# Kernel optimization log

Measured on AMD Instinct MI355X. Metric: run time of the kernel, lower is better.

The kernel has to match this reference:

```python
import jax, jax.numpy as jnp
import numpy as np


def setup_inputs() -> dict:
    key = jax.random.key(0)
    ks = jax.random.split(key, 7)
    B, H, W, C, HID = 8, 64, 64, 16, 256
    s = 0.05
    return {
        "x": jax.random.normal(ks[0], (B, H, W, C), jnp.float32),
        "W1": jax.random.normal(ks[1], (C, HID), jnp.float32) * s,
        "b1": jax.random.normal(ks[2], (C, HID), jnp.float32) * s,
        "W2": jax.random.normal(ks[3], (C, HID, HID), jnp.float32) * s,
        "b2": jax.random.normal(ks[4], (C, HID), jnp.float32) * s,
        "W3": jax.random.normal(ks[5], (C, HID, 3), jnp.float32) * s,
        "b3": jax.random.normal(ks[6], (C, 3), jnp.float32) * s,
    }


def reference(x, W1, b1, W2, b2, W3, b3):
    # x: [B,H,W,C] -> per-channel independent 3-layer MLP (1 -> HID -> HID -> 3)
    B, H, W, C = x.shape
    xf = x.reshape(-1, C)                                   # [N, C]
    # fc1: Linear(1, HID) per channel == scalar * weight + bias
    h = jax.nn.relu(xf[:, :, None] * W1[None] + b1[None])   # [N, C, HID]
    # fc2: batched GEMM over channels
    h = jax.nn.relu(jnp.einsum('nch,chk->nck', h, W2) + b2[None])  # [N, C, HID]
    # fc3: HID -> 3 per channel
    out = jnp.einsum('nch,cho->nco', h, W3) + b3[None]      # [N, C, 3]
    # torch.cat(outputs, dim=1) yields [c0_0..c0_2, c1_0..c1_2, ...] == reshape
    return out.reshape(B, H, W, C * 3)
```

## Files before the change

### kernel.cpp

```cpp
#include <hip/hip_runtime.h>
#include <hip/hip_bf16.h>


typedef __bf16 bf16_t;
typedef __attribute__((ext_vector_type(8))) __bf16 bf16x8;
typedef __attribute__((ext_vector_type(4))) __bf16 bf16x4;
typedef __attribute__((ext_vector_type(4))) float floatx4;

#define C_CH  16
#define HID   256
#define TILES 16
#define NSEG  257
#define GPTS  4097
#define XLO   (-6.0f)
#define XSTEP (12.0f / 4096.0f)

__device__ __forceinline__ unsigned mword(int i) {
  return 0x9E3779B1u + (unsigned)i * 0x85EBCA77u;
}

__global__ __launch_bounds__(512, 2) void kan_all(
    const float* __restrict__ x,
    const float* __restrict__ W1, const float* __restrict__ b1,
    const float* __restrict__ W2, const float* __restrict__ b2,
    const float* __restrict__ W3, const float* __restrict__ b3,
    bf16_t* __restrict__ tab, float* __restrict__ ftab,
    unsigned* __restrict__ flags, float* __restrict__ out) {
  __shared__ __align__(16) float tk[256];
  __shared__ float sW1[256], sB1[256];
  __shared__ int prank[2][256];
  __shared__ float caS[256], ccS[256];
  __shared__ float part[8][64][9];
  __shared__ float eA[17], eC[17];
  __shared__ int eH[17];
  __shared__ float tls[256];
  __shared__ short sjs[257];
  const int bid = blockIdx.x;
  const int c = bid & 15;
  const int k = bid >> 4;
  const int j0 = (NSEG * k) >> 4;
  const int j1 = (NSEG * (k + 1)) >> 4;
  const int nev = j1 - 1 - j0;
  const int t = threadIdx.x;

  if (t < 256) {
    float w = W1[c * 256 + t], bv = b1[c * 256 + t];
    sW1[t] = w;
    sB1[t] = bv;
    tk[t] = (w != 0.0f) ? (-bv / w) : 3.0e38f;
  }
  __syncthreads();
  {
    const int e = t & 255;
    const int hf = t >> 8;
    const float ke = tk[e];
    const int u0 = hf << 7;
    int r = 0;
#pragma unroll
    for (int uu = 0; uu < 32; ++uu) {
      const int u = u0 + uu * 4;
      const float4 kv = *(const float4*)&tk[u];
      r += (kv.x < ke || (kv.x == ke && (u + 0) < e)) ? 1 : 0;
      r += (kv.y < ke || (kv.y == ke && (u + 1) < e)) ? 1 : 0;
      r += (kv.z < ke || (kv.z == ke && (u + 2) < e)) ? 1 : 0;
      r += (kv.w < ke || (kv.w == ke && (u + 3) < e)) ? 1 : 0;
    }
    prank[hf][e] = r;
  }
  __syncthreads();
  if (t < 256) {
    const int r = prank[0][t] + prank[1][t];
    const float w = sW1[t], bv = sB1[t];
    tls[r] = tk[t];
    if (r >= j0 && r < j0 + nev) {
      const int e = r - j0;
      eA[e] = fabsf(w);
      eC[e] = (w > 0.f) ? bv : ((w < 0.f) ? -bv : 0.f);
      eH[e] = t;
    }
    bool act = (w > 0.f) ? (j0 > r) : ((w < 0.f) ? (j0 <= r) : (bv > 0.f));
    caS[t] = act ? w : 0.f;
    ccS[t] = act ? bv : 0.f;
  }
  __syncthreads();

  const int rg = t >> 6;
  const int q = t & 63;
  const float* W2c = W2 + ((size_t)c << 16);
  {
    float pa0 = 0.f, pa1 = 0.f, pa2 = 0.f, pa3 = 0.f;
    float pc0 = 0.f, pc1 = 0.f, pc2 = 0.f, pc3 = 0.f;
    for (int h0 = rg * 32; h0 < rg * 32 + 32; h0 += 8) {
      float4 v[8];
#pragma unroll
      for (int u = 0; u < 8; ++u)
        v[u] = *(const float4*)(W2c + (size_t)(h0 + u) * 256 + q * 4);
#pragma unroll
      for (int u = 0; u < 8; ++u) {
        float ca = caS[h0 + u], cc = ccS[h0 + u];
        pa0 = fmaf(ca, v[u].x, pa0); pa1 = fmaf(ca, v[u].y, pa1);
        pa2 = fmaf(ca, v[u].z, pa2); pa3 = fmaf(ca, v[u].w, pa3);
        pc0 = fmaf(cc, v[u].x, pc0); pc1 = fmaf(cc, v[u].y, pc1);
        pc2 = fmaf(cc, v[u].z, pc2); pc3 = fmaf(cc, v[u].w, pc3);
      }
    }
    part[rg][q][0] = pa0; part[rg][q][1] = pa1;
    part[rg][q][2] = pa2; part[rg][q][3] = pa3;
    part[rg][q][4] = pc0; part[rg][q][5] = pc1;
    part[rg][q][6] = pc2; part[rg][q][7] = pc3;
  }
  __syncthreads();

  if (t < 256) {
    float accA = 0.f, accC = b2[c * 256 + t];
    {
      const int qq = t >> 2, ii = t & 3;
#pragma unroll
      for (int rr = 0; rr < 8; ++rr) {
        accA += part[rr][qq][ii];
        accC += part[rr][qq][4 + ii];
      }
    }
    {
      bf16_t* rp = tab + ((size_t)c * NSEG + j0) * 512;
      rp[t] = (bf16_t)accA; rp[256 + t] = (bf16_t)accC;
    }

    float ew[16];
#pragma unroll 16
    for (int e = 0; e < 16; ++e)
      if (e < nev) ew[e] = W2c[eH[e] * 256 + t];
#pragma unroll 16
    for (int e = 0; e < 16; ++e) {
      if (e < nev) {
        accA = fmaf(eA[e], ew[e], accA);
        accC = fmaf(eC[e], ew[e], accC);
        bf16_t* rp = tab + ((size_t)c * NSEG + (j0 + 1 + e)) * 512;
        rp[t] = (bf16_t)accA; rp[256 + t] = (bf16_t)accC;
      }
    }
  }

  __syncthreads();
  if (t == 0) {
    __hip_atomic_store(&flags[c * 16 + k], mword(c * 16 + k),
                       __ATOMIC_RELEASE, __HIP_MEMORY_SCOPE_AGENT);
  }
  if (t < 16) {
    const int idx = c * 16 + t;
    const unsigned want = mword(idx);
    while (__hip_atomic_load(&flags[idx], __ATOMIC_RELAXED,
                             __HIP_MEMORY_SCOPE_AGENT) != want) {
      __builtin_amdgcn_s_sleep(4);
    }
  }
  if (t == 0) {
    (void)__hip_atomic_load(&flags[c * 16], __ATOMIC_ACQUIRE,
                            __HIP_MEMORY_SCOPE_AGENT);
  }
  __syncthreads();

  {
    const int gp0 = k << 8;
    const int l16 = t & 15;
    const int g = t >> 4;
    float w3f0[16], w3f1[16], w3f2[16];
#pragma unroll
    for (int u = 0; u < 16; ++u) {
      const float* wp = W3 + ((size_t)c * 256 + l16 * 16 + u) * 3;
      w3f0[u] = wp[0]; w3f1[u] = wp[1]; w3f2[u] = wp[2];
    }
    const float b3v0 = b3[c * 3 + 0], b3v1 = b3[c * 3 + 1], b3v2 = b3[c * 3 + 2];

    if (t < 257) {
      const int gp = gp0 + t;
      if (gp <= 4096) {
        const float xv = XLO + (float)gp * XSTEP;
        int j = 0;
#pragma unroll
        for (int s = 128; s > 0; s >>= 1)
          if (tls[j + s - 1] <= xv) j += s;
        if (j == 255 && tls[255] <= xv) j = 256;
        else if (j < 255 && tls[j] <= xv) ++j;
        sjs[t] = (short)j;
      } else {
        sjs[t] = 0;
      }
    }
    __syncthreads();

    const bf16_t* tabc = tab + (size_t)c * NSEG * 512;
    float xv = XLO + (float)(gp0 + g) * XSTEP;
    const bf16_t* row = tabc + (size_t)sjs[g] * 512 + l16 * 16;
    bf16x8 a0 = *(const bf16x8*)(row);
    bf16x8 a1 = *(const bf16x8*)(row + 8);
    bf16x8 c0 = *(const bf16x8*)(row + 256);
    bf16x8 c1 = *(const bf16x8*)(row + 264);

    for (int i = 0; i < 8; ++i) {
      bf16x8 na0, na1, nc0, nc1;
      float nxv = 0.f;
      if (i < 7) {
        int npl = (i + 1) * 32 + g;
        nxv = XLO + (float)(gp0 + npl) * XSTEP;
        const bf16_t* nrow = tabc + (size_t)sjs[npl] * 512 + l16 * 16;
        na0 = *(const bf16x8*)(nrow);
        na1 = *(const bf16x8*)(nrow + 8);
        nc0 = *(const bf16x8*)(nrow + 256);
        nc1 = *(const bf16x8*)(nrow + 264);
      }
      float s0 = 0.f, s1 = 0.f, s2 = 0.f;
#pragma unroll
      for (int u = 0; u < 8; ++u) {
        float h2 = fmaxf(fmaf(xv, (float)a0[u], (float)c0[u]), 0.f);
        s0 = fmaf(h2, w3f0[u], s0);
        s1 = fmaf(h2, w3f1[u], s1);
        s2 = fmaf(h2, w3f2[u], s2);
      }
#pragma unroll
      for (int u = 0; u < 8; ++u) {
        float h2 = fmaxf(fmaf(xv, (float)a1[u], (float)c1[u]), 0.f);
        s0 = fmaf(h2, w3f0[8 + u], s0);
        s1 = fmaf(h2, w3f1[8 + u], s1);
        s2 = fmaf(h2, w3f2[8 + u], s2);
      }
#pragma unroll
      for (int m = 1; m < 16; m <<= 1) {
        s0 += __shfl_xor(s0, m, 64);
        s1 += __shfl_xor(s1, m, 64);
        s2 += __shfl_xor(s2, m, 64);
      }
      const int gp = gp0 + i * 32 + g;
      if (l16 < 3) {
        float v = (l16 == 0) ? (s0 + b3v0) : (l16 == 1) ? (s1 + b3v1) : (s2 + b3v2);
        ftab[((size_t)c * GPTS + gp) * 4 + l16] = v;
      }
      a0 = na0; a1 = na1; c0 = nc0; c1 = nc1; xv = nxv;
    }

    if (k == 15 && t < 16) {
      const float xvt = XLO + 4096.0f * XSTEP;
      const bf16_t* rowt = tabc + (size_t)sjs[256] * 512 + t * 16;
      bf16x8 ta0 = *(const bf16x8*)(rowt);
      bf16x8 ta1 = *(const bf16x8*)(rowt + 8);
      bf16x8 tc0 = *(const bf16x8*)(rowt + 256);
      bf16x8 tc1 = *(const bf16x8*)(rowt + 264);
      float s0 = 0.f, s1 = 0.f, s2 = 0.f;
#pragma unroll
      for (int u = 0; u < 8; ++u) {
        float h2 = fmaxf(fmaf(xvt, (float)ta0[u], (float)tc0[u]), 0.f);
        s0 = fmaf(h2, w3f0[u], s0);
        s1 = fmaf(h2, w3f1[u], s1);
        s2 = fmaf(h2, w3f2[u], s2);
      }
#pragma unroll
      for (int u = 0; u < 8; ++u) {
        float h2 = fmaxf(fmaf(xvt, (float)ta1[u], (float)tc1[u]), 0.f);
        s0 = fmaf(h2, w3f0[8 + u], s0);
        s1 = fmaf(h2, w3f1[8 + u], s1);
        s2 = fmaf(h2, w3f2[8 + u], s2);
      }
#pragma unroll
      for (int m = 1; m < 16; m <<= 1) {
        s0 += __shfl_xor(s0, m, 64);
        s1 += __shfl_xor(s1, m, 64);
        s2 += __shfl_xor(s2, m, 64);
      }
      if (t < 3) {
        float v = (t == 0) ? (s0 + b3v0) : (t == 1) ? (s1 + b3v1) : (s2 + b3v2);
        ftab[((size_t)c * GPTS + 4096) * 4 + t] = v;
      }
    }
  }

  __syncthreads();
  if (t == 0) {
    __hip_atomic_store(&flags[256 + bid], mword(256 + bid),
                       __ATOMIC_RELEASE, __HIP_MEMORY_SCOPE_AGENT);
  }
  if (t < 256) {
    const int idx = 256 + t;
    const unsigned want = mword(idx);
    while (__hip_atomic_load(&flags[idx], __ATOMIC_RELAXED,
                             __HIP_MEMORY_SCOPE_AGENT) != want) {
      __builtin_amdgcn_s_sleep(4);
    }
  }
  if (t == 0) {
    (void)__hip_atomic_load(&flags[256], __ATOMIC_ACQUIRE,
                            __HIP_MEMORY_SCOPE_AGENT);
  }
  __syncthreads();

  {
    const int base3 = bid * 512 + t;
    const float inv = 1.0f / XSTEP;
    float xv4[4];
#pragma unroll
    for (int it = 0; it < 4; ++it) xv4[it] = x[it * 131072 + base3];
    float4 fa4[4], fb4[4];
    float f4[4];
#pragma unroll
    for (int it = 0; it < 4; ++it) {
      const int flat = it * 131072 + base3;
      const int cc = flat & 15;
      float u = (xv4[it] - XLO) * inv;
      int i = (int)floorf(u);
      i = i < 0 ? 0 : (i > 4095 ? 4095 : i);
      f4[it] = u - (float)i;
      const float4* fp = (const float4*)ftab + (size_t)cc * GPTS + i;
      fa4[it] = fp[0];
      fb4[it] = fp[1];
    }
#pragma unroll
    for (int it = 0; it < 4; ++it) {
      const int flat = it * 131072 + base3;
      float* op = out + (size_t)flat * 3;
      op[0] = fmaf(fb4[it].x - fa4[it].x, f4[it], fa4[it].x);
      op[1] = fmaf(fb4[it].y - fa4[it].y, f4[it], fa4[it].y);
      op[2] = fmaf(fb4[it].z - fa4[it].z, f4[it], fa4[it].z);
    }
  }
}

__global__ __launch_bounds__(512, 2) void build_tab(
    const float* __restrict__ W1, const float* __restrict__ b1,
    const float* __restrict__ W2, const float* __restrict__ b2,
    bf16_t* __restrict__ tab, float* __restrict__ ts_g) {
  __shared__ __align__(16) float tk[256];
  __shared__ float sW1[256], sB1[256];
  __shared__ int prank[2][256];
  __shared__ float caS[256], ccS[256];
  __shared__ float part[8][64][9];
  __shared__ float eA[17], eC[17];
  __shared__ int eH[17];
  const int c = blockIdx.x & 15;
  const int k = blockIdx.x >> 4;
  const int j0 = (NSEG * k) >> 4;
  const int j1 = (NSEG * (k + 1)) >> 4;
  const int nev = j1 - 1 - j0;
  const int t = threadIdx.x;

  if (t < 256) {
    float w = W1[c * 256 + t], bv = b1[c * 256 + t];
    sW1[t] = w;
    sB1[t] = bv;
    tk[t] = (w != 0.0f) ? (-bv / w) : 3.0e38f;
  }
  __syncthreads();
  {
    const int e = t & 255;
    const int hf = t >> 8;
    const float ke = tk[e];
    const int u0 = hf << 7;
    int r = 0;
#pragma unroll
    for (int uu = 0; uu < 32; ++uu) {
      const int u = u0 + uu * 4;
      const float4 kv = *(const float4*)&tk[u];
      r += (kv.x < ke || (kv.x == ke && (u + 0) < e)) ? 1 : 0;
      r += (kv.y < ke || (kv.y == ke && (u + 1) < e)) ? 1 : 0;
      r += (kv.z < ke || (kv.z == ke && (u + 2) < e)) ? 1 : 0;
      r += (kv.w < ke || (kv.w == ke && (u + 3) < e)) ? 1 : 0;
    }
    prank[hf][e] = r;
  }
  __syncthreads();
  if (t < 256) {
    const int r = prank[0][t] + prank[1][t];
    const float w = sW1[t], bv = sB1[t];
    if (k == 0) ts_g[c * 256 + r] = tk[t];
    if (r >= j0 && r < j0 + nev) {
      const int e = r - j0;
      eA[e] = fabsf(w);
      eC[e] = (w > 0.f) ? bv : ((w < 0.f) ? -bv : 0.f);
      eH[e] = t;
    }
    bool act = (w > 0.f) ? (j0 > r) : ((w < 0.f) ? (j0 <= r) : (bv > 0.f));
    caS[t] = act ? w : 0.f;
    ccS[t] = act ? bv : 0.f;
  }
  __syncthreads();

  const int rg = t >> 6;
  const int q = t & 63;
  const float* W2c = W2 + ((size_t)c << 16);
  float pa0 = 0.f, pa1 = 0.f, pa2 = 0.f, pa3 = 0.f;
  float pc0 = 0.f, pc1 = 0.f, pc2 = 0.f, pc3 = 0.f;
  for (int h0 = rg * 32; h0 < rg * 32 + 32; h0 += 8) {
    float4 v[8];
#pragma unroll
    for (int u = 0; u < 8; ++u)
      v[u] = *(const float4*)(W2c + (size_t)(h0 + u) * 256 + q * 4);
#pragma unroll
    for (int u = 0; u < 8; ++u) {
      float ca = caS[h0 + u], cc = ccS[h0 + u];
      pa0 = fmaf(ca, v[u].x, pa0); pa1 = fmaf(ca, v[u].y, pa1);
      pa2 = fmaf(ca, v[u].z, pa2); pa3 = fmaf(ca, v[u].w, pa3);
      pc0 = fmaf(cc, v[u].x, pc0); pc1 = fmaf(cc, v[u].y, pc1);
      pc2 = fmaf(cc, v[u].z, pc2); pc3 = fmaf(cc, v[u].w, pc3);
    }
  }
  part[rg][q][0] = pa0; part[rg][q][1] = pa1;
  part[rg][q][2] = pa2; part[rg][q][3] = pa3;
  part[rg][q][4] = pc0; part[rg][q][5] = pc1;
  part[rg][q][6] = pc2; part[rg][q][7] = pc3;
  __syncthreads();

  if (t < 256) {
    float accA = 0.f, accC = b2[c * 256 + t];
    {
      const int qq = t >> 2, ii = t & 3;
#pragma unroll
      for (int rr = 0; rr < 8; ++rr) {
        accA += part[rr][qq][ii];
        accC += part[rr][qq][4 + ii];
      }
    }
    {
      bf16_t* rp = tab + ((size_t)c * NSEG + j0) * 512;
      rp[t] = (bf16_t)accA; rp[256 + t] = (bf16_t)accC;
    }
    float ew[16];
#pragma unroll 16
    for (int e = 0; e < 16; ++e)
      if (e < nev) ew[e] = W2c[eH[e] * 256 + t];
#pragma unroll 16
    for (int e = 0; e < 16; ++e) {
      if (e < nev) {
        accA = fmaf(eA[e], ew[e], accA);
        accC = fmaf(eC[e], ew[e], accC);
        bf16_t* rp = tab + ((size_t)c * NSEG + (j0 + 1 + e)) * 512;
        rp[t] = (bf16_t)accA; rp[256 + t] = (bf16_t)accC;
      }
    }
  }
}

__global__ __launch_bounds__(256) void build_ftab(
    const bf16_t* __restrict__ tab, const float* __restrict__ ts_g,
    const float* __restrict__ W3, const float* __restrict__ b3,
    float* __restrict__ ftab) {
  __shared__ float tls[256];
  __shared__ short sj[64];
  const int t = threadIdx.x;
  const int c = blockIdx.x & 15;
  const int q = blockIdx.x >> 4;
  const int gp0 = q * 64;

  tls[t] = ts_g[c * 256 + t];

  const int l16 = t & 15;
  const int g = t >> 4;
  float w3f0[16], w3f1[16], w3f2[16];
#pragma unroll
  for (int u = 0; u < 16; ++u) {
    const float* wp = W3 + ((size_t)c * 256 + l16 * 16 + u) * 3;
    w3f0[u] = wp[0]; w3f1[u] = wp[1]; w3f2[u] = wp[2];
  }
  const float b3v0 = b3[c * 3 + 0], b3v1 = b3[c * 3 + 1], b3v2 = b3[c * 3 + 2];
  __syncthreads();

  if (t < 64) {
    const int gp = gp0 + t;
    if (gp <= 4096) {
      const float xv = XLO + (float)gp * XSTEP;
      int j = 0;
#pragma unroll
      for (int s = 128; s > 0; s >>= 1)
        if (tls[j + s - 1] <= xv) j += s;
      if (j == 255 && tls[255] <= xv) j = 256;
      else if (j < 255 && tls[j] <= xv) ++j;
      sj[t] = (short)j;
    } else {
      sj[t] = 0;
    }
  }
  __syncthreads();

  const bf16_t* tabc = tab + (size_t)c * NSEG * 512;
  float xv = XLO + (float)(gp0 + g) * XSTEP;
  const bf16_t* row = tabc + (size_t)sj[g] * 512 + l16 * 16;
  bf16x8 a0 = *(const bf16x8*)(row);
  bf16x8 a1 = *(const bf16x8*)(row + 8);
  bf16x8 c0 = *(const bf16x8*)(row + 256);
  bf16x8 c1 = *(const bf16x8*)(row + 264);

  for (int i = 0; i < 4; ++i) {
    bf16x8 na0, na1, nc0, nc1;
    float nxv = 0.f;
    if (i < 3) {
      int npl = (i + 1) * 16 + g;
      nxv = XLO + (float)(gp0 + npl) * XSTEP;
      const bf16_t* nrow = tabc + (size_t)sj[npl] * 512 + l16 * 16;
      na0 = *(const bf16x8*)(nrow);
      na1 = *(const bf16x8*)(nrow + 8);
      nc0 = *(const bf16x8*)(nrow + 256);
      nc1 = *(const bf16x8*)(nrow + 264);
    }
    float s0 = 0.f, s1 = 0.f, s2 = 0.f;
#pragma unroll
    for (int u = 0; u < 8; ++u) {
      float h2 = fmaxf(fmaf(xv, (float)a0[u], (float)c0[u]), 0.f);
      s0 = fmaf(h2, w3f0[u], s0);
      s1 = fmaf(h2, w3f1[u], s1);
      s2 = fmaf(h2, w3f2[u], s2);
    }
#pragma unroll
    for (int u = 0; u < 8; ++u) {
      float h2 = fmaxf(fmaf(xv, (float)a1[u], (float)c1[u]), 0.f);
      s0 = fmaf(h2, w3f0[8 + u], s0);
      s1 = fmaf(h2, w3f1[8 + u], s1);
      s2 = fmaf(h2, w3f2[8 + u], s2);
    }
#pragma unroll
    for (int m = 1; m < 16; m <<= 1) {
      s0 += __shfl_xor(s0, m, 64);
      s1 += __shfl_xor(s1, m, 64);
      s2 += __shfl_xor(s2, m, 64);
    }
    const int gp = gp0 + i * 16 + g;
    if (l16 < 3 && gp <= 4096) {
      float v = (l16 == 0) ? (s0 + b3v0) : (l16 == 1) ? (s1 + b3v1) : (s2 + b3v2);
      ftab[((size_t)c * GPTS + gp) * 4 + l16] = v;
    }
    a0 = na0; a1 = na1; c0 = nc0; c1 = nc1; xv = nxv;
  }
}

__global__ __launch_bounds__(256) void kan_eval(
    const float* __restrict__ x, const float* __restrict__ ftab,
    float* __restrict__ out) {
  const int flat = blockIdx.x * 256 + threadIdx.x;
  const float inv = 1.0f / XSTEP;
  const float xv = x[flat];
  const int c = flat & 15;
  float u = (xv - XLO) * inv;
  int i = (int)floorf(u);
  i = i < 0 ? 0 : (i > 4095 ? 4095 : i);
  const float f = u - (float)i;
  const float4* fp = (const float4*)ftab + (size_t)c * GPTS + i;
  float4 fa = fp[0];
  float4 fb = fp[1];
  float* op = out + (size_t)flat * 3;
  op[0] = fmaf(fb.x - fa.x, f, fa.x);
  op[1] = fmaf(fb.y - fa.y, f, fa.y);
  op[2] = fmaf(fb.z - fa.z, f, fa.z);
}

__global__ __launch_bounds__(256) void transpose_w2(const float* __restrict__ W2,
                                                    bf16_t* __restrict__ W2t) {
  __shared__ __align__(16) bf16_t tl[64][72];
  const int bid = blockIdx.x;
  const int c = bid >> 4, ti = (bid >> 2) & 3, tj = bid & 3;
  const int t = threadIdx.x;
  const float* src = W2 + (size_t)(c * 256 + tj * 64) * 256 + ti * 64;
#pragma unroll
  for (int it = 0; it < 4; ++it) {
    int idx = it * 256 + t;
    int h = idx >> 4, q = idx & 15;
    float4 v = *(const float4*)(src + h * 256 + q * 4);
    tl[h][q * 4 + 0] = (bf16_t)v.x;
    tl[h][q * 4 + 1] = (bf16_t)v.y;
    tl[h][q * 4 + 2] = (bf16_t)v.z;
    tl[h][q * 4 + 3] = (bf16_t)v.w;
  }
  __syncthreads();
  bf16_t* dst = W2t + (size_t)(c * 256 + ti * 64) * 256 + tj * 64;
#pragma unroll
  for (int it = 0; it < 2; ++it) {
    int idx = it * 256 + t;
    int n = idx >> 3, h8 = (idx & 7) * 8;
    bf16x8 tmp;
#pragma unroll
    for (int q = 0; q < 8; ++q) tmp[q] = tl[h8 + q][n];
    *(bf16x8*)(dst + n * 256 + h8) = tmp;
  }
}

template <bool DIRECT>
__global__ __launch_bounds__(256, 2) void kan_fused(
    const float* __restrict__ x, const float* __restrict__ W1,
    const float* __restrict__ b1, const bf16_t* __restrict__ W2t,
    const float* __restrict__ W2, const float* __restrict__ b2,
    const float* __restrict__ W3, const float* __restrict__ b3,
    float* __restrict__ out) {
  __shared__ __align__(16) bf16_t h1[64][264];
  __shared__ __align__(16) bf16_t w3t[4][288];
  const int t = threadIdx.x;
  const int lane = t & 63;
  const int wv = t >> 6;
  const int bid = blockIdx.x;
  const int c = bid & 15;
  const int g = bid >> 4;
  const int l15 = lane & 15;
  const int l4 = lane >> 4;
  const int nw0 = wv * 64;
  bf16x8 Bf[32];
  if (!DIRECT) {
    const bf16_t* Bbase = W2t + ((size_t)c << 16) + (size_t)(nw0 + l15) * HID + l4 * 8;
#pragma unroll
    for (int kt = 0; kt < 4; ++kt)
#pragma unroll
      for (int ks = 0; ks < 2; ++ks)
#pragma unroll
        for (int jn = 0; jn < 4; ++jn)
          Bf[kt * 8 + ks * 4 + jn] =
              *(const bf16x8*)(Bbase + jn * (16 * HID) + kt * 64 + ks * 32);
  } else {
#pragma unroll
    for (int kt = 0; kt < 4; ++kt)
#pragma unroll
      for (int ks = 0; ks < 2; ++ks)
#pragma unroll
        for (int jn = 0; jn < 4; ++jn) {
          const float* gp = W2 + ((size_t)c << 16) +
                            (size_t)(kt * 64 + ks * 32 + l4 * 8) * HID +
                            (nw0 + jn * 16 + l15);
#pragma unroll
          for (int j = 0; j < 8; ++j) Bf[kt * 8 + ks * 4 + jn][j] = (bf16_t)gp[j * HID];
        }
  }
  const int j8 = (t & 31) * 8;
  float wf[8], bf_[8];
  {
    float4 w0 = *(const float4*)(W1 + c * HID + j8);
    float4 w1v = *(const float4*)(W1 + c * HID + j8 + 4);
    float4 bb0 = *(const float4*)(b1 + c * HID + j8);
    float4 bb1 = *(const float4*)(b1 + c * HID + j8 + 4);
    wf[0] = w0.x; wf[1] = w0.y; wf[2] = w0.z; wf[3] = w0.w;
    wf[4] = w1v.x; wf[5] = w1v.y; wf[6] = w1v.z; wf[7] = w1v.w;
    bf_[0] = bb0.x; bf_[1] = bb0.y; bf_[2] = bb0.z; bf_[3] = bb0.w;
    bf_[4] = bb1.x; bf_[5] = bb1.y; bf_[6] = bb1.z; bf_[7] = bb1.w;
  }
  floatx4 b2v[4];
#pragma unroll
  for (int jn = 0; jn < 4; ++jn)
    b2v[jn] = *(const floatx4*)(b2 + c * HID + nw0 + jn * 16 + l4 * 4);
  const float b3v = b3[c * 3 + (l15 < 3 ? l15 : 0)];
  const int bhalf = (lane >> 5) & 1;
  w3t[0][t] = (bf16_t)W3[(c * HID + t) * 3 + 0];
  w3t[1][t] = (bf16_t)W3[(c * HID + t) * 3 + 1];
  w3t[2][t] = (bf16_t)W3[(c * HID + t) * 3 + 2];
  w3t[3][t] = (bf16_t)0.0f;
  const floatx4 zero4 = {0.f, 0.f, 0.f, 0.f};
  float xr = 0.0f;
  {
    int ml = (lane >> 1) * 8 + wv * 2 + (lane & 1);
    if (lane < 16) xr = x[(size_t)(g * TILES * 64 + ml) * C_CH + c];
  }
  for (int tile = 0; tile < TILES; ++tile) {
    const int m0 = (g * TILES + tile) * 64;
#pragma unroll
    for (int it = 0; it < 8; ++it) {
      int m = it * 8 + (t >> 5);
      float xm = __shfl(xr, it * 2 + bhalf, 64);
      bf16x8 hv;
#pragma unroll
      for (int q = 0; q < 8; ++q)
        hv[q] = (bf16_t)fmaxf(xm * wf[q] + bf_[q], 0.0f);
      *(bf16x8*)&h1[m][j8] = hv;
    }
    __syncthreads();
    float xr_n = 0.0f;
    if (tile + 1 < TILES && lane < 16) {
      int ml = (lane >> 1) * 8 + wv * 2 + (lane & 1);
      xr_n = x[(size_t)(m0 + 64 + ml) * C_CH + c];
    }
    floatx4 acc[4][4];
#pragma unroll
    for (int im = 0; im < 4; ++im)
#pragma unroll
      for (int jn = 0; jn < 4; ++jn) acc[im][jn] = zero4;
#pragma unroll
    for (int kt = 0; kt < 4; ++kt) {
#pragma unroll
      for (int ks = 0; ks < 2; ++ks) {
        const int k0 = kt * 64 + ks * 32;
        bf16x8 af[4];
#pragma unroll
        for (int im = 0; im < 4; ++im)
          af[im] = *(const bf16x8*)&h1[im * 16 + l15][k0 + l4 * 8];
#pragma unroll
        for (int im = 0; im < 4; ++im)
#pragma unroll
          for (int jn = 0; jn < 4; ++jn)
            acc[im][jn] = __builtin_amdgcn_mfma_f32_16x16x32_bf16(
                Bf[kt * 8 + ks * 4 + jn], af[im], acc[im][jn], 0, 0, 0);
      }
    }
    __syncthreads();
#pragma unroll
    for (int im = 0; im < 4; ++im)
#pragma unroll
      for (int jn = 0; jn < 4; ++jn) {
        bf16x4 hv;
#pragma unroll
        for (int r = 0; r < 4; ++r)
          hv[r] = (bf16_t)fmaxf(acc[im][jn][r] + b2v[jn][r], 0.0f);
        *(bf16x4*)&h1[im * 16 + l15][nw0 + jn * 16 + l4 * 4] = hv;
      }
    __syncthreads();
    {
      floatx4 acc3 = zero4;
      const int br = l15 < 3 ? l15 : 3;
#pragma unroll
      for (int kk = 0; kk < 8; ++kk) {
        bf16x8 a3 = *(const bf16x8*)&h1[wv * 16 + l15][kk * 32 + l4 * 8];
        bf16x8 bf3 = *(const bf16x8*)&w3t[br][kk * 32 + l4 * 8];
        acc3 = __builtin_amdgcn_mfma_f32_16x16x32_bf16(a3, bf3, acc3, 0, 0, 0);
      }
      if (l15 < 3) {
        float* op = out + ((size_t)((m0 + wv * 16 + l4 * 4) * C_CH + c) * 3) + l15;
#pragma unroll
        for (int r = 0; r < 4; ++r) op[r * (C_CH * 3)] = acc3[r] + b3v;
      }
    }
    __syncthreads();
    xr = xr_n;
  }
}

extern "C" void kernel_launch(void* const* d_in, const int* in_sizes, int n_in,
                              void* d_out, int out_size, void* d_ws, size_t ws_size,
                              hipStream_t stream) {
  const float* x = (const float*)d_in[0];
  const float* W1 = (const float*)d_in[1];
  const float* b1 = (const float*)d_in[2];
  const float* W2 = (const float*)d_in[3];
  const float* b2 = (const float*)d_in[4];
  const float* W3 = (const float*)d_in[5];
  const float* b3 = (const float*)d_in[6];
  float* out = (float*)d_out;

  const size_t tab_bytes = (size_t)C_CH * NSEG * 512 * sizeof(bf16_t);
  const size_t ftab_bytes = (size_t)C_CH * GPTS * 4 * sizeof(float);
  const size_t ts_bytes = (size_t)C_CH * 256 * sizeof(float);
  const size_t flag_bytes = 2048;
  if (ws_size >= tab_bytes + ftab_bytes + flag_bytes) {
    bf16_t* tab = (bf16_t*)d_ws;
    float* ftab = (float*)((char*)d_ws + tab_bytes);
    unsigned* flags = (unsigned*)((char*)d_ws + tab_bytes + ftab_bytes);
    kan_all<<<256, 512, 0, stream>>>(x, W1, b1, W2, b2, W3, b3, tab, ftab, flags, out);
  } else if (ws_size >= tab_bytes + ftab_bytes + ts_bytes) {
    bf16_t* tab = (bf16_t*)d_ws;
    float* ftab = (float*)((char*)d_ws + tab_bytes);
    float* ts_g = (float*)((char*)d_ws + tab_bytes + ftab_bytes);
    build_tab<<<256, 512, 0, stream>>>(W1, b1, W2, b2, tab, ts_g);
    build_ftab<<<1040, 256, 0, stream>>>(tab, ts_g, W3, b3, ftab);
    kan_eval<<<2048, 256, 0, stream>>>(x, ftab, out);
  } else if (ws_size >= (size_t)C_CH * HID * HID * sizeof(bf16_t)) {
    bf16_t* W2t = (bf16_t*)d_ws;
    transpose_w2<<<256, 256, 0, stream>>>(W2, W2t);
    kan_fused<false><<<512, 256, 0, stream>>>(x, W1, b1, W2t, W2, b2, W3, b3, out);
  } else {
    kan_fused<true><<<512, 256, 0, stream>>>(x, W1, b1, (bf16_t*)d_ws, W2, b2, W3, b3, out);
  }
}
```

Baseline: 105.7 us.

## Double block size, prefetch x early, and centralize the final grid barrier

Raises the kan_all block size from 512 to 1024 threads and re-splits the rank, W2 partial-sum, ftab and eval loops to match, so each block does fewer serial iterations. It also loads x at kernel start to hide latency, hoists the W3 register loads above the flag spin, and swaps the all-blocks-poll-256-flags barrier for one where block 0 gathers the flags and publishes a single flag. The intent is to cut grid-barrier polling traffic and the serial latency in each phase. In exchange, register pressure rises under the 1024-thread launch bound, and the single-flag barrier adds one extra hop of latency.

```diff
diff --git a/kernel.cpp b/kernel.cpp
--- a/kernel.cpp
+++ b/kernel.cpp
@@ -19,7 +19,7 @@
   return 0x9E3779B1u + (unsigned)i * 0x85EBCA77u;
 }
 
-__global__ __launch_bounds__(512, 2) void kan_all(
+__global__ __launch_bounds__(1024, 4) void kan_all(
     const float* __restrict__ x,
     const float* __restrict__ W1, const float* __restrict__ b1,
     const float* __restrict__ W2, const float* __restrict__ b2,
@@ -28,9 +28,9 @@
     unsigned* __restrict__ flags, float* __restrict__ out) {
   __shared__ __align__(16) float tk[256];
   __shared__ float sW1[256], sB1[256];
-  __shared__ int prank[2][256];
+  __shared__ int prank[4][256];
   __shared__ float caS[256], ccS[256];
-  __shared__ float part[8][64][9];
+  __shared__ float part[16][64][9];
   __shared__ float eA[17], eC[17];
   __shared__ int eH[17];
   __shared__ float tls[256];
@@ -43,6 +43,11 @@
   const int nev = j1 - 1 - j0;
   const int t = threadIdx.x;
 
+  const int base3 = bid * 1024 + t;
+  float xp0 = x[base3];
+  float xp1 = x[262144 + base3];
+  asm volatile("" :: "v"(xp0), "v"(xp1));
+
   if (t < 256) {
     float w = W1[c * 256 + t], bv = b1[c * 256 + t];
     sW1[t] = w;
@@ -52,12 +57,12 @@
   __syncthreads();
   {
     const int e = t & 255;
-    const int hf = t >> 8;
+    const int qf = t >> 8;
     const float ke = tk[e];
-    const int u0 = hf << 7;
+    const int u0 = qf << 6;
     int r = 0;
 #pragma unroll
-    for (int uu = 0; uu < 32; ++uu) {
+    for (int uu = 0; uu < 16; ++uu) {
       const int u = u0 + uu * 4;
       const float4 kv = *(const float4*)&tk[u];
       r += (kv.x < ke || (kv.x == ke && (u + 0) < e)) ? 1 : 0;
@@ -65,11 +70,11 @@
       r += (kv.z < ke || (kv.z == ke && (u + 2) < e)) ? 1 : 0;
       r += (kv.w < ke || (kv.w == ke && (u + 3) < e)) ? 1 : 0;
     }
-    prank[hf][e] = r;
+    prank[qf][e] = r;
   }
   __syncthreads();
   if (t < 256) {
-    const int r = prank[0][t] + prank[1][t];
+    const int r = prank[0][t] + prank[1][t] + prank[2][t] + prank[3][t];
     const float w = sW1[t], bv = sB1[t];
     tls[r] = tk[t];
     if (r >= j0 && r < j0 + nev) {
@@ -90,7 +95,7 @@
   {
     float pa0 = 0.f, pa1 = 0.f, pa2 = 0.f, pa3 = 0.f;
     float pc0 = 0.f, pc1 = 0.f, pc2 = 0.f, pc3 = 0.f;
-    for (int h0 = rg * 32; h0 < rg * 32 + 32; h0 += 8) {
+    for (int h0 = rg * 16; h0 < rg * 16 + 16; h0 += 8) {
       float4 v[8];
 #pragma unroll
       for (int u = 0; u < 8; ++u)
@@ -116,7 +121,7 @@
     {
       const int qq = t >> 2, ii = t & 3;
 #pragma unroll
-      for (int rr = 0; rr < 8; ++rr) {
+      for (int rr = 0; rr < 16; ++rr) {
         accA += part[rr][qq][ii];
         accC += part[rr][qq][4 + ii];
       }
@@ -146,6 +151,15 @@
     __hip_atomic_store(&flags[c * 16 + k], mword(c * 16 + k),
                        __ATOMIC_RELEASE, __HIP_MEMORY_SCOPE_AGENT);
   }
+  const int l16 = t & 15;
+  const int g = t >> 4;
+  float w3f0[16], w3f1[16], w3f2[16];
+#pragma unroll
+  for (int u = 0; u < 16; ++u) {
+    const float* wp = W3 + ((size_t)c * 256 + l16 * 16 + u) * 3;
+    w3f0[u] = wp[0]; w3f1[u] = wp[1]; w3f2[u] = wp[2];
+  }
+  const float b3v0 = b3[c * 3 + 0], b3v1 = b3[c * 3 + 1], b3v2 = b3[c * 3 + 2];
   if (t < 16) {
     const int idx = c * 16 + t;
     const unsigned want = mword(idx);
@@ -154,24 +168,12 @@
       __builtin_amdgcn_s_sleep(4);
     }
   }
-  if (t == 0) {
-    (void)__hip_atomic_load(&flags[c * 16], __ATOMIC_ACQUIRE,
-                            __HIP_MEMORY_SCOPE_AGENT);
-  }
+  __syncthreads();
+  if (t == 0) __builtin_amdgcn_fence(__ATOMIC_ACQUIRE, "agent");
   __syncthreads();
 
   {
     const int gp0 = k << 8;
-    const int l16 = t & 15;
-    const int g = t >> 4;
-    float w3f0[16], w3f1[16], w3f2[16];
-#pragma unroll
-    for (int u = 0; u < 16; ++u) {
-      const float* wp = W3 + ((size_t)c * 256 + l16 * 16 + u) * 3;
-      w3f0[u] = wp[0]; w3f1[u] = wp[1]; w3f2[u] = wp[2];
-    }
-    const float b3v0 = b3[c * 3 + 0], b3v1 = b3[c * 3 + 1], b3v2 = b3[c * 3 + 2];
-
     if (t < 257) {
       const int gp = gp0 + t;
       if (gp <= 4096) {
@@ -197,11 +199,11 @@
     bf16x8 c0 = *(const bf16x8*)(row + 256);
     bf16x8 c1 = *(const bf16x8*)(row + 264);
 
-    for (int i = 0; i < 8; ++i) {
+    for (int i = 0; i < 4; ++i) {
       bf16x8 na0, na1, nc0, nc1;
       float nxv = 0.f;
-      if (i < 7) {
-        int npl = (i + 1) * 32 + g;
+      if (i < 3) {
+        int npl = (i + 1) * 64 + g;
         nxv = XLO + (float)(gp0 + npl) * XSTEP;
         const bf16_t* nrow = tabc + (size_t)sjs[npl] * 512 + l16 * 16;
         na0 = *(const bf16x8*)(nrow);
@@ -230,7 +232,7 @@
         s1 += __shfl_xor(s1, m, 64);
         s2 += __shfl_xor(s2, m, 64);
       }
-      const int gp = gp0 + i * 32 + g;
+      const int gp = gp0 + i * 64 + g;
       if (l16 < 3) {
         float v = (l16 == 0) ? (s0 + b3v0) : (l16 == 1) ? (s1 + b3v1) : (s2 + b3v2);
         ftab[((size_t)c * GPTS + gp) * 4 + l16] = v;
@@ -278,48 +280,55 @@
     __hip_atomic_store(&flags[256 + bid], mword(256 + bid),
                        __ATOMIC_RELEASE, __HIP_MEMORY_SCOPE_AGENT);
   }
-  if (t < 256) {
-    const int idx = 256 + t;
-    const unsigned want = mword(idx);
-    while (__hip_atomic_load(&flags[idx], __ATOMIC_RELAXED,
+  if (bid == 0) {
+    if (t < 256) {
+      const int idx = 256 + t;
+      const unsigned want = mword(idx);
+      while (__hip_atomic_load(&flags[idx], __ATOMIC_RELAXED,
+                               __HIP_MEMORY_SCOPE_AGENT) != want) {
+        __builtin_amdgcn_s_sleep(4);
+      }
+    }
+    __syncthreads();
+    if (t == 0) {
+      __builtin_amdgcn_fence(__ATOMIC_ACQUIRE, "agent");
+      __hip_atomic_store(&flags[512], mword(512),
+                         __ATOMIC_RELEASE, __HIP_MEMORY_SCOPE_AGENT);
+    }
+  }
+  if (t == 0) {
+    const unsigned want = mword(512);
+    while (__hip_atomic_load(&flags[512], __ATOMIC_RELAXED,
                              __HIP_MEMORY_SCOPE_AGENT) != want) {
       __builtin_amdgcn_s_sleep(4);
     }
-  }
-  if (t == 0) {
-    (void)__hip_atomic_load(&flags[256], __ATOMIC_ACQUIRE,
-                            __HIP_MEMORY_SCOPE_AGENT);
+    __builtin_amdgcn_fence(__ATOMIC_ACQUIRE, "agent");
   }
   __syncthreads();
 
   {
-    const int base3 = bid * 512 + t;
     const float inv = 1.0f / XSTEP;
-    float xv4[4];
-#pragma unroll
-    for (int it = 0; it < 4; ++it) xv4[it] = x[it * 131072 + base3];
-    float4 fa4[4], fb4[4];
-    float f4[4];
-#pragma unroll
-    for (int it = 0; it < 4; ++it) {
-      const int flat = it * 131072 + base3;
-      const int cc = flat & 15;
-      float u = (xv4[it] - XLO) * inv;
-      int i = (int)floorf(u);
-      i = i < 0 ? 0 : (i > 4095 ? 4095 : i);
-      f4[it] = u - (float)i;
-      const float4* fp = (const float4*)ftab + (size_t)cc * GPTS + i;
-      fa4[it] = fp[0];
-      fb4[it] = fp[1];
-    }
-#pragma unroll
-    for (int it = 0; it < 4; ++it) {
-      const int flat = it * 131072 + base3;
-      float* op = out + (size_t)flat * 3;
-      op[0] = fmaf(fb4[it].x - fa4[it].x, f4[it], fa4[it].x);
-      op[1] = fmaf(fb4[it].y - fa4[it].y, f4[it], fa4[it].y);
-      op[2] = fmaf(fb4[it].z - fa4[it].z, f4[it], fa4[it].z);
-    }
+    const int cc = base3 & 15;
+    float u0 = (xp0 - XLO) * inv;
+    int i0 = (int)floorf(u0);
+    i0 = i0 < 0 ? 0 : (i0 > 4095 ? 4095 : i0);
+    const float f0 = u0 - (float)i0;
+    float u1 = (xp1 - XLO) * inv;
+    int i1 = (int)floorf(u1);
+    i1 = i1 < 0 ? 0 : (i1 > 4095 ? 4095 : i1);
+    const float f1 = u1 - (float)i1;
+    const float4* fp0 = (const float4*)ftab + (size_t)cc * GPTS + i0;
+    const float4* fp1 = (const float4*)ftab + (size_t)cc * GPTS + i1;
+    float4 fa0 = fp0[0], fb0 = fp0[1];
+    float4 fa1 = fp1[0], fb1 = fp1[1];
+    float* op0 = out + (size_t)base3 * 3;
+    op0[0] = fmaf(fb0.x - fa0.x, f0, fa0.x);
+    op0[1] = fmaf(fb0.y - fa0.y, f0, fa0.y);
+    op0[2] = fmaf(fb0.z - fa0.z, f0, fa0.z);
+    float* op1 = out + (size_t)(262144 + base3) * 3;
+    op1[0] = fmaf(fb1.x - fa1.x, f1, fa1.x);
+    op1[1] = fmaf(fb1.y - fa1.y, f1, fa1.y);
+    op1[2] = fmaf(fb1.z - fa1.z, f1, fa1.z);
   }
 }
 
@@ -736,12 +745,12 @@
   const size_t tab_bytes = (size_t)C_CH * NSEG * 512 * sizeof(bf16_t);
   const size_t ftab_bytes = (size_t)C_CH * GPTS * 4 * sizeof(float);
   const size_t ts_bytes = (size_t)C_CH * 256 * sizeof(float);
-  const size_t flag_bytes = 2048;
+  const size_t flag_bytes = 4096;
   if (ws_size >= tab_bytes + ftab_bytes + flag_bytes) {
     bf16_t* tab = (bf16_t*)d_ws;
     float* ftab = (float*)((char*)d_ws + tab_bytes);
     unsigned* flags = (unsigned*)((char*)d_ws + tab_bytes + ftab_bytes);
-    kan_all<<<256, 512, 0, stream>>>(x, W1, b1, W2, b2, W3, b3, tab, ftab, flags, out);
+    kan_all<<<256, 1024, 0, stream>>>(x, W1, b1, W2, b2, W3, b3, tab, ftab, flags, out);
   } else if (ws_size >= tab_bytes + ftab_bytes + ts_bytes) {
     bf16_t* tab = (bf16_t*)d_ws;
     float* ftab = (float*)((char*)d_ws + tab_bytes);
```

Result: faster. 100.4 us (-5.1%).
